# Performance work log

Measured on AMD Instinct MI355X. Metric: run time of the kernel, lower is better.

The kernel has to match this reference:

```python
import jax, jax.numpy as jnp
import numpy as np
import math

B, T, S, D, H = 2, 1024, 1024, 1024, 16
DH = D // H


def setup_inputs() -> dict:
    key = jax.random.key(0)
    ks = jax.random.split(key, 13)
    scale = 1.0 / math.sqrt(D)
    inp = {
        "q": jax.random.normal(ks[0], (B, T, D), jnp.float32),
        "k": jax.random.normal(ks[1], (B, S, D), jnp.float32),
        "v": jax.random.normal(ks[2], (B, S, D), jnp.float32),
        # causal mask: True means masked
        "attn_mask": jnp.broadcast_to(
            jnp.triu(jnp.ones((T, S), jnp.bool_), k=1)[None, None], (B, 1, T, S)
        ),
        "attn_bias": jax.random.normal(ks[3], (B, H, T, S), jnp.float32),
        "Wq": jax.random.normal(ks[4], (D, D), jnp.float32) * scale,
        "bq": jnp.zeros((D,), jnp.float32),
        "Wk": jax.random.normal(ks[5], (D, D), jnp.float32) * scale,
        "bk": jnp.zeros((D,), jnp.float32),
        "Wv": jax.random.normal(ks[6], (D, D), jnp.float32) * scale,
        "bv": jnp.zeros((D,), jnp.float32),
        "Wo": jax.random.normal(ks[7], (D, D), jnp.float32) * scale,
        "bo": jnp.zeros((D,), jnp.float32),
        "bias_scale": jnp.asarray(0.5, jnp.float32),
    }
    return inp


def reference(q, k, v, attn_mask, attn_bias, Wq, bq, Wk, bk, Wv, bv, Wo, bo, bias_scale):
    # projections (torch Linear convention: x @ W.T + b), split heads
    qh = (q @ Wq.T + bq).reshape(B, T, H, DH)   # (B,T,H,DH)
    kh = (k @ Wk.T + bk).reshape(B, S, H, DH)
    vh = (v @ Wv.T + bv).reshape(B, S, H, DH)

    scores = jnp.einsum("bthd,bshd->bhts", qh, kh) / math.sqrt(DH)  # (B,H,T,S)
    scores = jnp.clip(scores, -80.0, 80.0)
    scores = jnp.where(attn_mask, -jnp.inf, scores)  # mask broadcasts over H
    attn = jax.nn.softmax(scores, axis=-1)

    # post-softmax multiplicative bias + renormalize
    scale = 1.0 + bias_scale * jnp.tanh(attn_bias)
    attn = attn * jnp.maximum(scale, 1e-9)
    attn = attn / (jnp.sum(attn, axis=-1, keepdims=True) + 1e-9)

    # dropout p=0.0 (eval) -> identity
    out = jnp.einsum("bhts,bshd->bthd", attn, vh).reshape(B, T, D)
    out = out @ Wo.T + bo
    return out, attn
```

## Files before the change

### kernel.cpp

```cpp
#include <hip/hip_runtime.h>
#include <hip/hip_bf16.h>
#include <math.h>

#define BB 2
#define TT 1024
#define SS 1024
#define DD 1024
#define HH 16
#define DH 64

typedef __attribute__((ext_vector_type(8))) short bf16x8;
typedef __attribute__((ext_vector_type(4))) float f32x4;
typedef unsigned short ushort_t;

#define AS3(p) ((__attribute__((address_space(3))) unsigned int*)(p))
#define AS1(p) ((const __attribute__((address_space(1))) unsigned int*)(p))

__device__ __forceinline__ unsigned short f2b(float f) {
    union { float f; unsigned u; } x; x.f = f;
    unsigned r = x.u + 0x7FFFu + ((x.u >> 16) & 1u);
    return (unsigned short)(r >> 16);
}

__device__ __forceinline__ bf16x8 pack_bf16x8(float4 a, float4 b) {
    union { unsigned u[4]; bf16x8 v; } r;
    asm("v_cvt_pk_bf16_f32 %0, %1, %2" : "=v"(r.u[0]) : "v"(a.x), "v"(a.y));
    asm("v_cvt_pk_bf16_f32 %0, %1, %2" : "=v"(r.u[1]) : "v"(a.z), "v"(a.w));
    asm("v_cvt_pk_bf16_f32 %0, %1, %2" : "=v"(r.u[2]) : "v"(b.x), "v"(b.y));
    asm("v_cvt_pk_bf16_f32 %0, %1, %2" : "=v"(r.u[3]) : "v"(b.z), "v"(b.w));
    return r.v;
}

__global__ __launch_bounds__(256) void cvt_all(
    const float* __restrict__ q, const float* __restrict__ k, const float* __restrict__ v,
    const float* __restrict__ Wq, const float* __restrict__ Wk,
    const float* __restrict__ Wv, const float* __restrict__ Wo,
    ushort_t* __restrict__ oq, ushort_t* __restrict__ ok, ushort_t* __restrict__ ov,
    ushort_t* __restrict__ oWq, ushort_t* __restrict__ oWk,
    ushort_t* __restrict__ oWv, ushort_t* __restrict__ oWo)
{
    const int y = blockIdx.y;
    if (y >= 3 && blockIdx.x >= 512) return;
    const float* src =
        (y == 0) ? q : (y == 1) ? k : (y == 2) ? v :
        (y == 3) ? Wq : (y == 4) ? Wk : (y == 5) ? Wv : Wo;
    ushort_t* dst =
        (y == 0) ? oq : (y == 1) ? ok : (y == 2) ? ov :
        (y == 3) ? oWq : (y == 4) ? oWk : (y == 5) ? oWv : oWo;
    size_t i = ((size_t)blockIdx.x * 256 + threadIdx.x) * 8;
    float4 v0 = *(const float4*)&src[i];
    float4 v1 = *(const float4*)&src[i + 4];
    uint4 o;
    o.x = f2b(v0.x) | ((unsigned)f2b(v0.y) << 16);
    o.y = f2b(v0.z) | ((unsigned)f2b(v0.w) << 16);
    o.z = f2b(v1.x) | ((unsigned)f2b(v1.y) << 16);
    o.w = f2b(v1.z) | ((unsigned)f2b(v1.w) << 16);
    *(uint4*)&dst[i] = o;
}

__device__ __forceinline__ void gemm128_mainloop(
    const ushort_t* __restrict__ A,
    const ushort_t* __restrict__ Bw,
    int K, ushort_t (*Asm)[128 * 32], ushort_t (*Bsm)[128 * 32],
    f32x4 acc[4][4])
{
    const int tid = threadIdx.x;
    const int wave = tid >> 6, lane = tid & 63;
    const int sr = lane >> 2;
    const int gc = (lane & 3) ^ ((lane >> 3) & 3);
    const int l15 = lane & 15, q = lane >> 4;
    const int mblk = (wave >> 1) * 64, nblk = (wave & 1) * 64;

#define G128_STAGE(k0_, b_) do {                                               \
        _Pragma("unroll")                                                      \
        for (int o = 0; o < 2; o++) {                                          \
            int r0 = (wave * 2 + o) * 16;                                      \
            __builtin_amdgcn_global_load_lds(                                  \
                AS1(A + (size_t)(r0 + sr) * K + (k0_) + gc * 8),               \
                AS3(Asm[b_] + r0 * 32), 16, 0, 0);                             \
            __builtin_amdgcn_global_load_lds(                                  \
                AS1(Bw + (size_t)(r0 + sr) * K + (k0_) + gc * 8),              \
                AS3(Bsm[b_] + r0 * 32), 16, 0, 0);                             \
        } } while (0)

#define G128_COMPUTE(b_) do {                                                  \
        bf16x8 av[4], bv[4];                                                   \
        _Pragma("unroll")                                                      \
        for (int mi = 0; mi < 4; mi++) {                                       \
            int r = mblk + mi * 16 + l15;                                      \
            av[mi] = *(const bf16x8*)&Asm[b_][r * 32 + (q ^ ((r >> 1) & 3)) * 8]; \
        }                                                                      \
        _Pragma("unroll")                                                      \
        for (int ni = 0; ni < 4; ni++) {                                       \
            int r = nblk + ni * 16 + l15;                                      \
            bv[ni] = *(const bf16x8*)&Bsm[b_][r * 32 + (q ^ ((r >> 1) & 3)) * 8]; \
        }                                                                      \
        _Pragma("unroll")                                                      \
        for (int mi = 0; mi < 4; mi++)                                         \
            _Pragma("unroll")                                                  \
            for (int ni = 0; ni < 4; ni++)                                     \
                acc[mi][ni] = __builtin_amdgcn_mfma_f32_16x16x32_bf16(         \
                    av[mi], bv[ni], acc[mi][ni], 0, 0, 0);                     \
        } while (0)

    G128_STAGE(0, 0);
    __syncthreads();

    int buf = 0;
    for (int k0 = 0; k0 < K; k0 += 32) {
        if (k0 + 32 < K) G128_STAGE(k0 + 32, buf ^ 1);
        G128_COMPUTE(buf);
        __syncthreads();
        buf ^= 1;
    }
#undef G128_STAGE
#undef G128_COMPUTE
}

__global__ __launch_bounds__(256) void proj_gemm(
    const ushort_t* __restrict__ qb, const ushort_t* __restrict__ kb, const ushort_t* __restrict__ vb,
    const ushort_t* __restrict__ Wqb, const ushort_t* __restrict__ Wkb, const ushort_t* __restrict__ Wvb,
    const float* __restrict__ bq, const float* __restrict__ bk, const float* __restrict__ bv,
    ushort_t* __restrict__ qh, ushort_t* __restrict__ kh, ushort_t* __restrict__ vh)
{
    __shared__ ushort_t Asm[2][128 * 32];
    __shared__ ushort_t Bsm[2][128 * 32];
    const int z = blockIdx.z;
    const ushort_t* A = (z == 0) ? qb : (z == 1) ? kb : vb;
    const ushort_t* W = (z == 0) ? Wqb : (z == 1) ? Wkb : Wvb;
    const float* bias = (z == 0) ? bq : (z == 1) ? bk : bv;
    ushort_t* Y = (z == 0) ? qh : (z == 1) ? kh : vh;

    const int bm = blockIdx.y * 128, bn = blockIdx.x * 128;
    f32x4 acc[4][4];
    #pragma unroll
    for (int i = 0; i < 4; i++)
        #pragma unroll
        for (int j = 0; j < 4; j++) acc[i][j] = (f32x4)(0.f);

    gemm128_mainloop(A + (size_t)bm * DD, W + (size_t)bn * DD, DD, Asm, Bsm, acc);

    const int lane = threadIdx.x & 63, wave = threadIdx.x >> 6;
    const int mblk = (wave >> 1) * 64, nblk = (wave & 1) * 64;
    const int l15 = lane & 15, q = lane >> 4;
    #pragma unroll
    for (int mi = 0; mi < 4; mi++) {
        #pragma unroll
        for (int ni = 0; ni < 4; ni++) {
            int col = bn + nblk + ni * 16 + l15;
            float bcol = bias[col];
            #pragma unroll
            for (int r = 0; r < 4; r++) {
                int row = bm + mblk + mi * 16 + q * 4 + r;
                Y[(size_t)row * DD + col] = f2b(acc[mi][ni][r] + bcol);
            }
        }
    }
}

__global__ __launch_bounds__(256) void oproj_gemm(
    const ushort_t* __restrict__ A, const ushort_t* __restrict__ W,
    const float* __restrict__ bias, float* __restrict__ Y)
{
    __shared__ ushort_t Asm[2][128 * 32];
    __shared__ ushort_t Bsm[2][128 * 32];
    const int bm = blockIdx.y * 128, bn = blockIdx.x * 128;
    f32x4 acc[4][4];
    #pragma unroll
    for (int i = 0; i < 4; i++)
        #pragma unroll
        for (int j = 0; j < 4; j++) acc[i][j] = (f32x4)(0.f);

    gemm128_mainloop(A + (size_t)bm * DD, W + (size_t)bn * DD, DD, Asm, Bsm, acc);

    const int lane = threadIdx.x & 63, wave = threadIdx.x >> 6;
    const int mblk = (wave >> 1) * 64, nblk = (wave & 1) * 64;
    const int l15 = lane & 15, q = lane >> 4;
    #pragma unroll
    for (int mi = 0; mi < 4; mi++) {
        #pragma unroll
        for (int ni = 0; ni < 4; ni++) {
            int col = bn + nblk + ni * 16 + l15;
            float bcol = bias[col];
            #pragma unroll
            for (int r = 0; r < 4; r++) {
                int row = bm + mblk + mi * 16 + q * 4 + r;
                Y[(size_t)row * DD + col] = acc[mi][ni][r] + bcol;
            }
        }
    }
}

__global__ __launch_bounds__(256) void transpose_v(
    const ushort_t* __restrict__ vh, ushort_t* __restrict__ vT)
{
    __shared__ ushort_t Ls[64][72];
    const int s0 = blockIdx.x * 64;
    const int bh = blockIdx.y;
    const int b = bh >> 4, h = bh & 15;
    const int tid = threadIdx.x;
    const int r = tid >> 2, c16 = (tid & 3) * 16;

    const ushort_t* src = &vh[((size_t)(b * SS + s0 + r) * HH + h) * DH + c16];
    uint4 u0 = *(const uint4*)src;
    uint4 u1 = *(const uint4*)(src + 8);
    ushort_t tmp[16];
    *(uint4*)&tmp[0] = u0; *(uint4*)&tmp[8] = u1;
    #pragma unroll
    for (int j = 0; j < 16; j++) Ls[c16 + j][r] = tmp[j];
    __syncthreads();

    const int dh = r;
    uint4 w0 = *(const uint4*)&Ls[dh][c16];
    uint4 w1 = *(const uint4*)&Ls[dh][c16 + 8];
    ushort_t* dst = &vT[((size_t)bh * DH + dh) * SS + s0 + c16];
    *(uint4*)dst = w0;
    *(uint4*)(dst + 8) = w1;
}

__global__ __launch_bounds__(256) void scores_mfma(
    const ushort_t* __restrict__ qh, const ushort_t* __restrict__ kh,
    float* __restrict__ attn)
{
    __shared__ ushort_t Qs[128 * 64];
    __shared__ ushort_t Ks[128 * 64];

    int idx = blockIdx.x, ti = 0;
    while (idx >= ti + 1) { idx -= ti + 1; ti++; }
    const int si = idx;
    const int bh = blockIdx.y;
    const int b = bh >> 4, h = bh & 15;
    const int t0 = ti * 128, s0 = si * 128;

    const int tid = threadIdx.x;
    const int wave = tid >> 6, lane = tid & 63;
    const int sr8 = lane >> 3;
    const int gc8 = (lane & 7) ^ sr8;

    #pragma unroll
    for (int o = 0; o < 4; o++) {
        int r0 = (wave * 4 + o) * 8;
        int r = r0 + sr8;
        __builtin_amdgcn_global_load_lds(
            AS1(qh + ((size_t)(b * TT + t0 + r) * HH + h) * DH + gc8 * 8),
            AS3(Qs + r0 * 64), 16, 0, 0);
        __builtin_amdgcn_global_load_lds(
            AS1(kh + ((size_t)(b * SS + s0 + r) * HH + h) * DH + gc8 * 8),
            AS3(Ks + r0 * 64), 16, 0, 0);
    }
    __syncthreads();

    const int l15 = lane & 15, q = lane >> 4;
    const int tblk = (wave >> 1) * 64, sblk = (wave & 1) * 64;
    f32x4 acc[4][4];
    #pragma unroll
    for (int i = 0; i < 4; i++)
        #pragma unroll
        for (int j = 0; j < 4; j++) acc[i][j] = (f32x4)(0.f);

    #pragma unroll
    for (int ks = 0; ks < 2; ks++) {
        bf16x8 av[4], bv[4];
        #pragma unroll
        for (int mi = 0; mi < 4; mi++) {
            int r = tblk + mi * 16 + l15;
            av[mi] = *(const bf16x8*)&Qs[r * 64 + ((ks * 4 + q) ^ (r & 7)) * 8];
        }
        #pragma unroll
        for (int ni = 0; ni < 4; ni++) {
            int r = sblk + ni * 16 + l15;
            bv[ni] = *(const bf16x8*)&Ks[r * 64 + ((ks * 4 + q) ^ (r & 7)) * 8];
        }
        #pragma unroll
        for (int mi = 0; mi < 4; mi++)
            #pragma unroll
            for (int ni = 0; ni < 4; ni++)
                acc[mi][ni] = __builtin_amdgcn_mfma_f32_16x16x32_bf16(av[mi], bv[ni], acc[mi][ni], 0, 0, 0);
    }

    #pragma unroll
    for (int mi = 0; mi < 4; mi++) {
        #pragma unroll
        for (int ni = 0; ni < 4; ni++) {
            int scol = s0 + sblk + ni * 16 + l15;
            #pragma unroll
            for (int r = 0; r < 4; r++) {
                int t = t0 + tblk + mi * 16 + q * 4 + r;
                float v = acc[mi][ni][r] * 0.125f;
                v = fminf(fmaxf(v, -80.f), 80.f);
                attn[((size_t)bh * TT + t) * SS + scol] = v;
            }
        }
    }
}

__global__ __launch_bounds__(256) void softmax_bias_wave(
    const float* __restrict__ attn_bias, const float* __restrict__ bias_scale_p,
    float* __restrict__ attn)
{
    const int wave = threadIdx.x >> 6, lane = threadIdx.x & 63;
    const int row = blockIdx.x * 4 + wave;
    const int t = row & (TT - 1);

    float* prow = attn + (size_t)row * SS;
    const float* brow = attn_bias + (size_t)row * SS;
    const float bscale = bias_scale_p[0];

    const int nc = (t >> 8) + 1;

    float v[16];
    float4 bx[4];
    float m = -INFINITY;
    #pragma unroll
    for (int c = 0; c < 4; c++) {
        const int s0 = c * 256 + lane * 4;
        if (c < nc) {
            float4 rv = *(const float4*)&prow[s0];
            bx[c] = *(const float4*)&brow[s0];
            v[c * 4 + 0] = (s0     <= t) ? rv.x : -INFINITY;
            v[c * 4 + 1] = (s0 + 1 <= t) ? rv.y : -INFINITY;
            v[c * 4 + 2] = (s0 + 2 <= t) ? rv.z : -INFINITY;
            v[c * 4 + 3] = (s0 + 3 <= t) ? rv.w : -INFINITY;
            m = fmaxf(m, fmaxf(fmaxf(v[c*4], v[c*4+1]), fmaxf(v[c*4+2], v[c*4+3])));
        } else {
            v[c * 4 + 0] = -INFINITY; v[c * 4 + 1] = -INFINITY;
            v[c * 4 + 2] = -INFINITY; v[c * 4 + 3] = -INFINITY;
            bx[c] = make_float4(0.f, 0.f, 0.f, 0.f);
        }
    }
    #pragma unroll
    for (int off = 1; off < 64; off <<= 1)
        m = fmaxf(m, __shfl_xor(m, off));

    float w[16];
    float P = 0.f, Wn = 0.f;
    #pragma unroll
    for (int c = 0; c < 4; c++) {
        if (c < nc) {
            float bxx[4] = {bx[c].x, bx[c].y, bx[c].z, bx[c].w};
            #pragma unroll
            for (int j = 0; j < 4; j++) {
                float vv = v[c * 4 + j];
                float p = (vv > -INFINITY) ? __expf(vv - m) : 0.f;
                float e = __expf(-2.f * fabsf(bxx[j]));
                float th = copysignf((1.f - e) / (1.f + e), bxx[j]);
                float sc = fmaxf(1.f + bscale * th, 1e-9f);
                float ww = p * sc;
                w[c * 4 + j] = ww;
                P += p; Wn += ww;
            }
        } else {
            w[c * 4 + 0] = 0.f; w[c * 4 + 1] = 0.f;
            w[c * 4 + 2] = 0.f; w[c * 4 + 3] = 0.f;
        }
    }
    #pragma unroll
    for (int off = 1; off < 64; off <<= 1) {
        P  += __shfl_xor(P, off);
        Wn += __shfl_xor(Wn, off);
    }
    const float inv = 1.f / (Wn + 1e-9f * P);

    #pragma unroll
    for (int c = 0; c < 4; c++) {
        const int s0 = c * 256 + lane * 4;
        float4 o;
        o.x = w[c * 4 + 0] * inv; o.y = w[c * 4 + 1] * inv;
        o.z = w[c * 4 + 2] * inv; o.w = w[c * 4 + 3] * inv;
        *(float4*)&prow[s0] = o;
    }
}

__global__ __launch_bounds__(256) void av_mfma(
    const float* __restrict__ attn, const ushort_t* __restrict__ vT,
    ushort_t* __restrict__ ao)
{
    __shared__ ushort_t Vsm[2][64 * 64];

    const int tb = (int)gridDim.x - 1 - (int)blockIdx.x;
    const int bh = blockIdx.y;
    const int b = bh >> 4, h = bh & 15;
    const int t0 = tb * 64;
    const int nsteps = tb + 1;

    const int tid = threadIdx.x;
    const int wave = tid >> 6, lane = tid & 63;
    const int sr8 = lane >> 3, gc8 = (lane & 7) ^ sr8;
    const int l15 = lane & 15, q = lane >> 4;

    const float* arow = attn + ((size_t)bh * TT + t0 + wave * 16 + l15) * SS + q * 8;
    const ushort_t* vbase = vT + (size_t)bh * DH * SS;

    f32x4 acc[4];
    #pragma unroll
    for (int i = 0; i < 4; i++) acc[i] = (f32x4)(0.f);

#define STAGE_V(sidx, buf) do {                                               \
        int s0_ = (sidx) * 64;                                                \
        _Pragma("unroll")                                                     \
        for (int o = 0; o < 2; o++) {                                         \
            int r0 = wave * 16 + o * 8;                                       \
            __builtin_amdgcn_global_load_lds(                                 \
                AS1(vbase + (size_t)(r0 + sr8) * SS + s0_ + gc8 * 8),         \
                AS3(&Vsm[buf][r0 * 64]), 16, 0, 0);                           \
        } } while (0)

#define LOAD_A(sidx, dst) do {                                                \
        const float* p_ = arow + (sidx) * 64;                                 \
        dst[0] = *(const float4*)(p_);                                        \
        dst[1] = *(const float4*)(p_ + 4);                                    \
        dst[2] = *(const float4*)(p_ + 32);                                   \
        dst[3] = *(const float4*)(p_ + 36); } while (0)

#define COMPUTE(buf, ax) do {                                                 \
        bf16x8 af0 = pack_bf16x8(ax[0], ax[1]);                               \
        bf16x8 af1 = pack_bf16x8(ax[2], ax[3]);                               \
        _Pragma("unroll")                                                     \
        for (int ni = 0; ni < 4; ni++) {                                      \
            int rv = ni * 16 + l15;                                           \
            bf16x8 b0 = *(const bf16x8*)&Vsm[buf][rv * 64 + ((q) ^ (rv & 7)) * 8];       \
            bf16x8 b1 = *(const bf16x8*)&Vsm[buf][rv * 64 + ((4 + q) ^ (rv & 7)) * 8];   \
            acc[ni] = __builtin_amdgcn_mfma_f32_16x16x32_bf16(af0, b0, acc[ni], 0, 0, 0);\
            acc[ni] = __builtin_amdgcn_mfma_f32_16x16x32_bf16(af1, b1, acc[ni], 0, 0, 0);\
        } } while (0)

    float4 aA[4], aB[4];
    STAGE_V(0, 0);
    LOAD_A(0, aA);
    __syncthreads();

    int st = 0;
    while (true) {
        if (st + 1 < nsteps) { STAGE_V(st + 1, 1); LOAD_A(st + 1, aB); }
        COMPUTE(0, aA);
        __syncthreads();
        if (++st == nsteps) break;
        if (st + 1 < nsteps) { STAGE_V(st + 1, 0); LOAD_A(st + 1, aA); }
        COMPUTE(1, aB);
        __syncthreads();
        if (++st == nsteps) break;
    }

#undef STAGE_V
#undef LOAD_A
#undef COMPUTE

    #pragma unroll
    for (int ni = 0; ni < 4; ni++) {
        int dh = ni * 16 + l15;
        #pragma unroll
        for (int r = 0; r < 4; r++) {
            int t = t0 + wave * 16 + q * 4 + r;
            ao[(size_t)(b * TT + t) * DD + h * DH + dh] = f2b(acc[ni][r]);
        }
    }
}

extern "C" void kernel_launch(void* const* d_in, const int* in_sizes, int n_in,
                              void* d_out, int out_size, void* d_ws, size_t ws_size,
                              hipStream_t stream)
{
    const float* q   = (const float*)d_in[0];
    const float* k   = (const float*)d_in[1];
    const float* v   = (const float*)d_in[2];
    const float* attn_bias = (const float*)d_in[4];
    const float* Wq = (const float*)d_in[5];
    const float* bq = (const float*)d_in[6];
    const float* Wk = (const float*)d_in[7];
    const float* bk = (const float*)d_in[8];
    const float* Wv = (const float*)d_in[9];
    const float* bv = (const float*)d_in[10];
    const float* Wo = (const float*)d_in[11];
    const float* bo = (const float*)d_in[12];
    const float* bscale = (const float*)d_in[13];

    char* base = (char*)d_ws;
    ushort_t* qb  = (ushort_t*)(base + (0ull << 20));
    ushort_t* kb  = (ushort_t*)(base + (4ull << 20));
    ushort_t* vb  = (ushort_t*)(base + (8ull << 20));
    ushort_t* Wqb = (ushort_t*)(base + (12ull << 20));
    ushort_t* Wkb = (ushort_t*)(base + (14ull << 20));
    ushort_t* Wvb = (ushort_t*)(base + (16ull << 20));
    ushort_t* Wob = (ushort_t*)(base + (18ull << 20));
    ushort_t* qhb = (ushort_t*)(base + (20ull << 20));
    ushort_t* khb = (ushort_t*)(base + (24ull << 20));
    ushort_t* vhb = (ushort_t*)(base + (28ull << 20));
    ushort_t* vT  = qb;
    ushort_t* aob = kb;

    float* out  = (float*)d_out;
    float* attn = out + (size_t)BB * TT * DD;

    cvt_all<<<dim3(1024, 7), 256, 0, stream>>>(q, k, v, Wq, Wk, Wv, Wo,
                                               qb, kb, vb, Wqb, Wkb, Wvb, Wob);
    proj_gemm<<<dim3(8, 16, 3), 256, 0, stream>>>(qb, kb, vb, Wqb, Wkb, Wvb,
                                                  bq, bk, bv, qhb, khb, vhb);
    transpose_v<<<dim3(16, 32), 256, 0, stream>>>(vhb, vT);
    scores_mfma<<<dim3(36, 32), 256, 0, stream>>>(qhb, khb, attn);
    softmax_bias_wave<<<dim3(8192), 256, 0, stream>>>(attn_bias, bscale, attn);
    av_mfma<<<dim3(16, 32), 256, 0, stream>>>(attn, vT, aob);
    oproj_gemm<<<dim3(8, 16), 256, 0, stream>>>(aob, Wob, bo, out);
}
```

Before: 367.4 us.

## Fuse V transpose into projection, deepen GEMM K-tile, drop softmax max pass

```diff
diff --git a/kernel.cpp b/kernel.cpp
--- a/kernel.cpp
+++ b/kernel.cpp
@@ -61,54 +61,56 @@
 __device__ __forceinline__ void gemm128_mainloop(
     const ushort_t* __restrict__ A,
     const ushort_t* __restrict__ Bw,
-    int K, ushort_t (*Asm)[128 * 32], ushort_t (*Bsm)[128 * 32],
+    int K, ushort_t (*Asm)[128 * 64], ushort_t (*Bsm)[128 * 64],
     f32x4 acc[4][4])
 {
     const int tid = threadIdx.x;
     const int wave = tid >> 6, lane = tid & 63;
-    const int sr = lane >> 2;
-    const int gc = (lane & 3) ^ ((lane >> 3) & 3);
+    const int sr8 = lane >> 3;
+    const int gc8 = (lane & 7) ^ sr8;
     const int l15 = lane & 15, q = lane >> 4;
     const int mblk = (wave >> 1) * 64, nblk = (wave & 1) * 64;
 
 #define G128_STAGE(k0_, b_) do {                                               \
         _Pragma("unroll")                                                      \
-        for (int o = 0; o < 2; o++) {                                          \
-            int r0 = (wave * 2 + o) * 16;                                      \
+        for (int o = 0; o < 4; o++) {                                          \
+            int r0 = wave * 32 + o * 8;                                        \
             __builtin_amdgcn_global_load_lds(                                  \
-                AS1(A + (size_t)(r0 + sr) * K + (k0_) + gc * 8),               \
-                AS3(Asm[b_] + r0 * 32), 16, 0, 0);                             \
+                AS1(A + (size_t)(r0 + sr8) * K + (k0_) + gc8 * 8),             \
+                AS3(Asm[b_] + r0 * 64), 16, 0, 0);                             \
             __builtin_amdgcn_global_load_lds(                                  \
-                AS1(Bw + (size_t)(r0 + sr) * K + (k0_) + gc * 8),              \
-                AS3(Bsm[b_] + r0 * 32), 16, 0, 0);                             \
+                AS1(Bw + (size_t)(r0 + sr8) * K + (k0_) + gc8 * 8),            \
+                AS3(Bsm[b_] + r0 * 64), 16, 0, 0);                             \
         } } while (0)
 
 #define G128_COMPUTE(b_) do {                                                  \
-        bf16x8 av[4], bv[4];                                                   \
         _Pragma("unroll")                                                      \
-        for (int mi = 0; mi < 4; mi++) {                                       \
-            int r = mblk + mi * 16 + l15;                                      \
-            av[mi] = *(const bf16x8*)&Asm[b_][r * 32 + (q ^ ((r >> 1) & 3)) * 8]; \
-        }                                                                      \
-        _Pragma("unroll")                                                      \
-        for (int ni = 0; ni < 4; ni++) {                                       \
-            int r = nblk + ni * 16 + l15;                                      \
-            bv[ni] = *(const bf16x8*)&Bsm[b_][r * 32 + (q ^ ((r >> 1) & 3)) * 8]; \
-        }                                                                      \
-        _Pragma("unroll")                                                      \
-        for (int mi = 0; mi < 4; mi++)                                         \
+        for (int ks = 0; ks < 2; ks++) {                                       \
+            bf16x8 av[4], bv[4];                                               \
             _Pragma("unroll")                                                  \
-            for (int ni = 0; ni < 4; ni++)                                     \
-                acc[mi][ni] = __builtin_amdgcn_mfma_f32_16x16x32_bf16(         \
-                    av[mi], bv[ni], acc[mi][ni], 0, 0, 0);                     \
-        } while (0)
+            for (int mi = 0; mi < 4; mi++) {                                   \
+                int r = mblk + mi * 16 + l15;                                  \
+                av[mi] = *(const bf16x8*)&Asm[b_][r * 64 + ((ks * 4 + q) ^ (r & 7)) * 8]; \
+            }                                                                  \
+            _Pragma("unroll")                                                  \
+            for (int ni = 0; ni < 4; ni++) {                                   \
+                int r = nblk + ni * 16 + l15;                                  \
+                bv[ni] = *(const bf16x8*)&Bsm[b_][r * 64 + ((ks * 4 + q) ^ (r & 7)) * 8]; \
+            }                                                                  \
+            _Pragma("unroll")                                                  \
+            for (int mi = 0; mi < 4; mi++)                                     \
+                _Pragma("unroll")                                              \
+                for (int ni = 0; ni < 4; ni++)                                 \
+                    acc[mi][ni] = __builtin_amdgcn_mfma_f32_16x16x32_bf16(     \
+                        av[mi], bv[ni], acc[mi][ni], 0, 0, 0);                 \
+        } } while (0)
 
     G128_STAGE(0, 0);
     __syncthreads();
 
     int buf = 0;
-    for (int k0 = 0; k0 < K; k0 += 32) {
-        if (k0 + 32 < K) G128_STAGE(k0 + 32, buf ^ 1);
+    for (int k0 = 0; k0 < K; k0 += 64) {
+        if (k0 + 64 < K) G128_STAGE(k0 + 64, buf ^ 1);
         G128_COMPUTE(buf);
         __syncthreads();
         buf ^= 1;
@@ -121,15 +123,14 @@
     const ushort_t* __restrict__ qb, const ushort_t* __restrict__ kb, const ushort_t* __restrict__ vb,
     const ushort_t* __restrict__ Wqb, const ushort_t* __restrict__ Wkb, const ushort_t* __restrict__ Wvb,
     const float* __restrict__ bq, const float* __restrict__ bk, const float* __restrict__ bv,
-    ushort_t* __restrict__ qh, ushort_t* __restrict__ kh, ushort_t* __restrict__ vh)
-{
-    __shared__ ushort_t Asm[2][128 * 32];
-    __shared__ ushort_t Bsm[2][128 * 32];
+    ushort_t* __restrict__ qh, ushort_t* __restrict__ kh, ushort_t* __restrict__ vT)
+{
+    __shared__ ushort_t Asm[2][128 * 64];
+    __shared__ ushort_t Bsm[2][128 * 64];
     const int z = blockIdx.z;
     const ushort_t* A = (z == 0) ? qb : (z == 1) ? kb : vb;
     const ushort_t* W = (z == 0) ? Wqb : (z == 1) ? Wkb : Wvb;
     const float* bias = (z == 0) ? bq : (z == 1) ? bk : bv;
-    ushort_t* Y = (z == 0) ? qh : (z == 1) ? kh : vh;
 
     const int bm = blockIdx.y * 128, bn = blockIdx.x * 128;
     f32x4 acc[4][4];
@@ -143,16 +144,39 @@
     const int lane = threadIdx.x & 63, wave = threadIdx.x >> 6;
     const int mblk = (wave >> 1) * 64, nblk = (wave & 1) * 64;
     const int l15 = lane & 15, q = lane >> 4;
-    #pragma unroll
-    for (int mi = 0; mi < 4; mi++) {
-        #pragma unroll
-        for (int ni = 0; ni < 4; ni++) {
-            int col = bn + nblk + ni * 16 + l15;
-            float bcol = bias[col];
-            #pragma unroll
-            for (int r = 0; r < 4; r++) {
-                int row = bm + mblk + mi * 16 + q * 4 + r;
-                Y[(size_t)row * DD + col] = f2b(acc[mi][ni][r] + bcol);
+
+    if (z < 2) {
+        ushort_t* Y = (z == 0) ? qh : kh;
+        #pragma unroll
+        for (int mi = 0; mi < 4; mi++) {
+            #pragma unroll
+            for (int ni = 0; ni < 4; ni++) {
+                int col = bn + nblk + ni * 16 + l15;
+                float bcol = bias[col];
+                #pragma unroll
+                for (int r = 0; r < 4; r++) {
+                    int row = bm + mblk + mi * 16 + q * 4 + r;
+                    Y[(size_t)row * DD + col] = f2b(acc[mi][ni][r] + bcol);
+                }
+            }
+        }
+    } else {
+        #pragma unroll
+        for (int mi = 0; mi < 4; mi++) {
+            int row0 = bm + mblk + mi * 16 + q * 4;
+            int b_ = row0 >> 10, s0_ = row0 & 1023;
+            #pragma unroll
+            for (int ni = 0; ni < 4; ni++) {
+                int col = bn + nblk + ni * 16 + l15;
+                float bcol = bias[col];
+                int h_ = col >> 6, dh_ = col & 63;
+                union { unsigned u[2]; } pk;
+                pk.u[0] = (unsigned)f2b(acc[mi][ni][0] + bcol)
+                        | ((unsigned)f2b(acc[mi][ni][1] + bcol) << 16);
+                pk.u[1] = (unsigned)f2b(acc[mi][ni][2] + bcol)
+                        | ((unsigned)f2b(acc[mi][ni][3] + bcol) << 16);
+                *(uint2*)&vT[((size_t)(b_ * 16 + h_) * 64 + dh_) * SS + s0_] =
+                    make_uint2(pk.u[0], pk.u[1]);
             }
         }
     }
@@ -162,8 +186,8 @@
     const ushort_t* __restrict__ A, const ushort_t* __restrict__ W,
     const float* __restrict__ bias, float* __restrict__ Y)
 {
-    __shared__ ushort_t Asm[2][128 * 32];
-    __shared__ ushort_t Bsm[2][128 * 32];
+    __shared__ ushort_t Asm[2][128 * 64];
+    __shared__ ushort_t Bsm[2][128 * 64];
     const int bm = blockIdx.y * 128, bn = blockIdx.x * 128;
     f32x4 acc[4][4];
     #pragma unroll
@@ -189,33 +213,6 @@
             }
         }
     }
-}
-
-__global__ __launch_bounds__(256) void transpose_v(
-    const ushort_t* __restrict__ vh, ushort_t* __restrict__ vT)
-{
-    __shared__ ushort_t Ls[64][72];
-    const int s0 = blockIdx.x * 64;
-    const int bh = blockIdx.y;
-    const int b = bh >> 4, h = bh & 15;
-    const int tid = threadIdx.x;
-    const int r = tid >> 2, c16 = (tid & 3) * 16;
-
-    const ushort_t* src = &vh[((size_t)(b * SS + s0 + r) * HH + h) * DH + c16];
-    uint4 u0 = *(const uint4*)src;
-    uint4 u1 = *(const uint4*)(src + 8);
-    ushort_t tmp[16];
-    *(uint4*)&tmp[0] = u0; *(uint4*)&tmp[8] = u1;
-    #pragma unroll
-    for (int j = 0; j < 16; j++) Ls[c16 + j][r] = tmp[j];
-    __syncthreads();
-
-    const int dh = r;
-    uint4 w0 = *(const uint4*)&Ls[dh][c16];
-    uint4 w1 = *(const uint4*)&Ls[dh][c16 + 8];
-    ushort_t* dst = &vT[((size_t)bh * DH + dh) * SS + s0 + c16];
-    *(uint4*)dst = w0;
-    *(uint4*)(dst + 8) = w1;
 }
 
 __global__ __launch_bounds__(256) void scores_mfma(
@@ -308,42 +305,21 @@
 
     const int nc = (t >> 8) + 1;
 
-    float v[16];
-    float4 bx[4];
-    float m = -INFINITY;
+    float w[16];
+    float P = 0.f, Wn = 0.f;
     #pragma unroll
     for (int c = 0; c < 4; c++) {
         const int s0 = c * 256 + lane * 4;
         if (c < nc) {
             float4 rv = *(const float4*)&prow[s0];
-            bx[c] = *(const float4*)&brow[s0];
-            v[c * 4 + 0] = (s0     <= t) ? rv.x : -INFINITY;
-            v[c * 4 + 1] = (s0 + 1 <= t) ? rv.y : -INFINITY;
-            v[c * 4 + 2] = (s0 + 2 <= t) ? rv.z : -INFINITY;
-            v[c * 4 + 3] = (s0 + 3 <= t) ? rv.w : -INFINITY;
-            m = fmaxf(m, fmaxf(fmaxf(v[c*4], v[c*4+1]), fmaxf(v[c*4+2], v[c*4+3])));
-        } else {
-            v[c * 4 + 0] = -INFINITY; v[c * 4 + 1] = -INFINITY;
-            v[c * 4 + 2] = -INFINITY; v[c * 4 + 3] = -INFINITY;
-            bx[c] = make_float4(0.f, 0.f, 0.f, 0.f);
-        }
-    }
-    #pragma unroll
-    for (int off = 1; off < 64; off <<= 1)
-        m = fmaxf(m, __shfl_xor(m, off));
-
-    float w[16];
-    float P = 0.f, Wn = 0.f;
-    #pragma unroll
-    for (int c = 0; c < 4; c++) {
-        if (c < nc) {
-            float bxx[4] = {bx[c].x, bx[c].y, bx[c].z, bx[c].w};
+            float4 bv = *(const float4*)&brow[s0];
+            float sv[4] = {rv.x, rv.y, rv.z, rv.w};
+            float bx[4] = {bv.x, bv.y, bv.z, bv.w};
             #pragma unroll
             for (int j = 0; j < 4; j++) {
-                float vv = v[c * 4 + j];
-                float p = (vv > -INFINITY) ? __expf(vv - m) : 0.f;
-                float e = __expf(-2.f * fabsf(bxx[j]));
-                float th = copysignf((1.f - e) / (1.f + e), bxx[j]);
+                float p = (s0 + j <= t) ? __expf(sv[j] - 16.f) : 0.f;
+                float e = __expf(-2.f * fabsf(bx[j]));
+                float th = copysignf((1.f - e) / (1.f + e), bx[j]);
                 float sc = fmaxf(1.f + bscale * th, 1e-9f);
                 float ww = p * sc;
                 w[c * 4 + j] = ww;
@@ -484,8 +460,7 @@
     ushort_t* Wob = (ushort_t*)(base + (18ull << 20));
     ushort_t* qhb = (ushort_t*)(base + (20ull << 20));
     ushort_t* khb = (ushort_t*)(base + (24ull << 20));
-    ushort_t* vhb = (ushort_t*)(base + (28ull << 20));
-    ushort_t* vT  = qb;
+    ushort_t* vT  = (ushort_t*)(base + (28ull << 20));
     ushort_t* aob = kb;
 
     float* out  = (float*)d_out;
@@ -494,8 +469,7 @@
     cvt_all<<<dim3(1024, 7), 256, 0, stream>>>(q, k, v, Wq, Wk, Wv, Wo,
                                                qb, kb, vb, Wqb, Wkb, Wvb, Wob);
     proj_gemm<<<dim3(8, 16, 3), 256, 0, stream>>>(qb, kb, vb, Wqb, Wkb, Wvb,
-                                                  bq, bk, bv, qhb, khb, vhb);
-    transpose_v<<<dim3(16, 32), 256, 0, stream>>>(vhb, vT);
+                                                  bq, bk, bv, qhb, khb, vT);
     scores_mfma<<<dim3(36, 32), 256, 0, stream>>>(qhb, khb, attn);
     softmax_bias_wave<<<dim3(8192), 256, 0, stream>>>(attn_bias, bscale, attn);
     av_mfma<<<dim3(16, 32), 256, 0, stream>>>(attn, vT, aob);
```

New measurement: 366.0 us. About the same (-0.4%).
